# Performance work log

Measured on AMD Instinct MI355X. Metric: run time of the kernel, lower is better.

The kernel has to match this reference:

```python
import jax, jax.numpy as jnp
import numpy as np

EPSILON = 8.0        # Gibbs kernel temperature (JCPOTConfig.epsilon)
NUM_INNER_ITER = 10  # Sinkhorn u/v fixed-point iterations
STAB = 1e-8          # denominator stabilizer, matches torch code


def _cost_matrix(s, t):
    # Euclidean pairwise distance, same math as torch.norm(s[:,None]-t[None,:], dim=2)
    # computed without materializing the [n_s, n_t, d] tensor.
    sq = jnp.sum(s * s, axis=1)[:, None] + jnp.sum(t * t, axis=1)[None, :] - 2.0 * (s @ t.T)
    return jnp.sqrt(jnp.maximum(sq, 0.0))


def setup_inputs() -> dict:
    key = jax.random.key(0)
    k1, k2 = jax.random.split(key)
    return {
        "source_features": jax.random.normal(k1, (4096, 512), dtype=jnp.float32),
        "target_features": jax.random.normal(k2, (4096, 512), dtype=jnp.float32),
    }


def reference(source_features, target_features):
    n_s = source_features.shape[0]
    n_t = target_features.shape[0]
    C = _cost_matrix(source_features, target_features)   # [n_s, n_t]
    K = jnp.exp(-C / EPSILON)                             # Gibbs kernel

    # uniform marginals (JCPOT passes uniform weights; Sinkhorn renormalizes -> same)
    a = jnp.full((n_s, 1), 1.0 / n_s, dtype=C.dtype)
    b = jnp.full((n_t, 1), 1.0 / n_t, dtype=C.dtype)

    def body(carry, _):
        u, v = carry
        u = a / (K @ v + STAB)
        v = b / (K.T @ u + STAB)
        return (u, v), None

    u0 = jnp.ones((n_s, 1), dtype=C.dtype)
    v0 = jnp.ones((n_t, 1), dtype=C.dtype)
    (u, v), _ = jax.lax.scan(body, (u0, v0), None, length=NUM_INNER_ITER)

    coupling = u * K * v.T                                # [n_s, n_t]
    ot_loss = jnp.sum(coupling * C) / (n_s * n_t)         # reduction='mean'
    # returns same contents as the torch dict: ot_loss, coupling, cost_matrix
    return ot_loss, coupling, C
```

## Files before the change

### kernel.cpp

```cpp
#include <hip/hip_runtime.h>
#include <math.h>


#define N_S 4096
#define N_T 4096
#define DIM 512
#define STAB 1e-8f

typedef _Float16 f16x2 __attribute__((ext_vector_type(2)));
typedef _Float16 f16x4 __attribute__((ext_vector_type(4)));
typedef _Float16 f16x8 __attribute__((ext_vector_type(8)));
typedef float f32x4v __attribute__((ext_vector_type(4)));

__global__ __launch_bounds__(256) void k_norms(const float4* __restrict__ S4,
                                               const float4* __restrict__ T4,
                                               float* __restrict__ ns, float* __restrict__ nt) {
    int t = threadIdx.x;
    int lane = t & 63, wave = t >> 6;
    int wid = blockIdx.x * 4 + wave;
    const float4* src; float* dst; int row;
    if (wid < N_S) { src = S4; dst = ns; row = wid; }
    else           { src = T4; dst = nt; row = wid - N_S; }
    float acc = 0.f;
#pragma unroll
    for (int c = 0; c < 2; ++c) {
        float4 x = src[row * 128 + c * 64 + lane];
        acc += x.x*x.x + x.y*x.y + x.z*x.z + x.w*x.w;
    }
#pragma unroll
    for (int m = 32; m; m >>= 1) acc += __shfl_xor(acc, m);
    if (lane == 0) dst[row] = acc;
}

__global__ void k_init(float* v, float* vacc, double* lossd) {
    int g = blockIdx.x * 256 + threadIdx.x;
    if (g < N_T) { v[g] = 1.0f; vacc[g] = 0.0f; }
    if (g == 0) *lossd = 0.0;
}

template<int MODE>
__global__ __launch_bounds__(256) void k_gemm(const float* __restrict__ S, const float* __restrict__ T,
                                              const float* __restrict__ ns, const float* __restrict__ nt,
                                              float* __restrict__ outK, _Float16* __restrict__ outKh,
                                              float* __restrict__ outC) {
    __shared__ _Float16 As[128 * 40];
    __shared__ _Float16 Bs[128 * 40];
    int t = threadIdx.x;
    int lane = t & 63, wave = t >> 6;
    int wr = wave >> 1, wc = wave & 1;
    int brow = blockIdx.x * 128, bcol = blockIdx.y * 128;

    f32x4v acc[4][4] = {};

    for (int kt = 0; kt < DIM; kt += 32) {
        __syncthreads();
#pragma unroll
        for (int w = 0; w < 4; ++w) {
            int e = w * 1024 + t * 4;
            int row = e >> 5, col = e & 31;
            float4 a = *(const float4*)(S + (size_t)(brow + row) * DIM + kt + col);
            f16x4 ah = { (_Float16)a.x, (_Float16)a.y, (_Float16)a.z, (_Float16)a.w };
            *(f16x4*)(&As[row * 40 + col]) = ah;
            float4 b = *(const float4*)(T + (size_t)(bcol + row) * DIM + kt + col);
            f16x4 bh = { (_Float16)b.x, (_Float16)b.y, (_Float16)b.z, (_Float16)b.w };
            *(f16x4*)(&Bs[row * 40 + col]) = bh;
        }
        __syncthreads();

        f16x8 af[4], bf[4];
#pragma unroll
        for (int m = 0; m < 4; ++m)
            af[m] = *(const f16x8*)(&As[(wr * 64 + m * 16 + (lane & 15)) * 40 + (lane >> 4) * 8]);
#pragma unroll
        for (int n = 0; n < 4; ++n)
            bf[n] = *(const f16x8*)(&Bs[(wc * 64 + n * 16 + (lane & 15)) * 40 + (lane >> 4) * 8]);
#pragma unroll
        for (int m = 0; m < 4; ++m)
#pragma unroll
            for (int n = 0; n < 4; ++n)
                acc[m][n] = __builtin_amdgcn_mfma_f32_16x16x32_f16(af[m], bf[n], acc[m][n], 0, 0, 0);
    }

#pragma unroll
    for (int m = 0; m < 4; ++m) {
#pragma unroll
        for (int n = 0; n < 4; ++n) {
#pragma unroll
            for (int r = 0; r < 4; ++r) {
                int i = brow + wr * 64 + m * 16 + (lane >> 4) * 4 + r;
                int j = bcol + wc * 64 + n * 16 + (lane & 15);
                float dot = acc[m][n][r];
                float sq = ns[i] + nt[j] - 2.0f * dot;
                float c = sqrtf(fmaxf(sq, 0.0f));
                float k = __expf(-c * 0.125f);
                size_t idx = (size_t)i * N_T + j;
                outC[idx] = c;
                if constexpr (MODE == 0) outK[idx] = k;
                else                     outKh[idx] = (_Float16)k;
            }
        }
    }
}

__global__ __launch_bounds__(256) void k_sink(const _Float16* __restrict__ Kh,
                                              const float* __restrict__ v,
                                              float* __restrict__ u_out,
                                              float* __restrict__ part) {
    __shared__ _Float16 rows[4][4096];
    __shared__ float u_s[4];
    int t = threadIdx.x, lane = t & 63, w = t >> 6;
    float2 acc[8];
#pragma unroll
    for (int s = 0; s < 8; ++s) acc[s] = make_float2(0.f, 0.f);

    for (int c = 0; c < 2; ++c) {
        if (c) __syncthreads();
        int row = blockIdx.x * 8 + c * 4 + w;
        const _Float16* Kr = Kh + (size_t)row * N_T;
        float dot = 0.f;
#pragma unroll
        for (int it = 0; it < 8; ++it) {
            int j0 = it * 512 + lane * 8;
            f16x8 kv = *(const f16x8*)(Kr + j0);
            float4 v0 = *(const float4*)(v + j0);
            float4 v1 = *(const float4*)(v + j0 + 4);
            *(f16x8*)(&rows[w][j0]) = kv;
            dot += (float)kv[0]*v0.x + (float)kv[1]*v0.y + (float)kv[2]*v0.z + (float)kv[3]*v0.w
                 + (float)kv[4]*v1.x + (float)kv[5]*v1.y + (float)kv[6]*v1.z + (float)kv[7]*v1.w;
        }
#pragma unroll
        for (int m = 32; m; m >>= 1) dot += __shfl_xor(dot, m);
        if (lane == 0) {
            float uv = (1.0f / N_S) / (dot + STAB);
            u_s[w] = uv;
            u_out[row] = uv;
        }
        __syncthreads();
#pragma unroll
        for (int s = 0; s < 8; ++s) {
            int jj = t * 2 + s * 512;
#pragma unroll
            for (int r = 0; r < 4; ++r) {
                f16x2 kk = *(const f16x2*)(&rows[r][jj]);
                float uu = u_s[r];
                acc[s].x += uu * (float)kk[0];
                acc[s].y += uu * (float)kk[1];
            }
        }
    }
    float* pb = part + (size_t)blockIdx.x * N_T;
#pragma unroll
    for (int s = 0; s < 8; ++s)
        *(float2*)(pb + t * 2 + s * 512) = acc[s];
}

__global__ __launch_bounds__(256) void k_vfin2(const float* __restrict__ part, float* __restrict__ v) {
    __shared__ float sums[256];
    int t = threadIdx.x;
    int jl = t & 15, c = t >> 4;
    int j = blockIdx.x * 16 + jl;
    float acc = 0.f;
#pragma unroll 8
    for (int k = 0; k < 32; ++k)
        acc += part[(size_t)(c * 32 + k) * N_T + j];
    sums[t] = acc;
    __syncthreads();
    if (t < 16) {
        float s = 0.f;
#pragma unroll
        for (int c2 = 0; c2 < 16; ++c2) s += sums[c2 * 16 + t];
        v[blockIdx.x * 16 + t] = (1.0f / N_T) / (s + STAB);
    }
}

__global__ __launch_bounds__(256) void k_final2(const _Float16* __restrict__ Kh, const float* __restrict__ Cd,
                                                const float* __restrict__ u, const float* __restrict__ v,
                                                float* __restrict__ W, double* __restrict__ lossd) {
    int t = threadIdx.x, row = blockIdx.x;
    float ui = u[row];
    float lacc = 0.f;
    const _Float16* Kr = Kh + (size_t)row * N_T;
    const float* Cr = Cd + (size_t)row * N_T;
    float* Wr = W + (size_t)row * N_T;
#pragma unroll
    for (int cc = 0; cc < 4; ++cc) {
        int j = (cc * 256 + t) * 4;
        f16x4 kk = *(const f16x4*)(Kr + j);
        float4 c4 = *(const float4*)(Cr + j);
        float4 v4 = *(const float4*)(v + j);
        float4 w4;
        w4.x = ui * (float)kk[0] * v4.x;
        w4.y = ui * (float)kk[1] * v4.y;
        w4.z = ui * (float)kk[2] * v4.z;
        w4.w = ui * (float)kk[3] * v4.w;
        *(float4*)(Wr + j) = w4;
        lacc += w4.x*c4.x + w4.y*c4.y + w4.z*c4.z + w4.w*c4.w;
    }
#pragma unroll
    for (int m = 32; m; m >>= 1) lacc += __shfl_xor(lacc, m);
    __shared__ float wsum[4];
    int lane = t & 63, wave = t >> 6;
    if (lane == 0) wsum[wave] = lacc;
    __syncthreads();
    if (t == 0) atomicAdd(lossd, (double)(wsum[0] + wsum[1] + wsum[2] + wsum[3]));
}

__global__ void k_loss(const double* __restrict__ lossd, float* __restrict__ out0) {
    *out0 = (float)(*lossd / ((double)N_S * (double)N_T));
}

__global__ __launch_bounds__(256) void k_rowmv(const float* __restrict__ Kd,
                                               const float* __restrict__ v, float* __restrict__ u) {
    __shared__ float vl[4096];
    int t = threadIdx.x;
#pragma unroll
    for (int c = 0; c < 16; ++c) vl[c * 256 + t] = v[c * 256 + t];
    __syncthreads();
    int lane = t & 63, wave = t >> 6;
    int row = blockIdx.x * 4 + wave;
    const float* Kr = Kd + (size_t)row * N_T;
    float dot = 0.f;
#pragma unroll 8
    for (int c = 0; c < 64; ++c) {
        int j = c * 64 + lane;
        dot += Kr[j] * vl[j];
    }
#pragma unroll
    for (int m = 32; m; m >>= 1) dot += __shfl_xor(dot, m);
    if (lane == 0) u[row] = (1.0f / N_S) / (dot + STAB);
}

__global__ __launch_bounds__(256) void k_colmv(const float* __restrict__ Kd,
                                               const float* __restrict__ u, float* __restrict__ vacc) {
    __shared__ float ul[64];
    int t = threadIdx.x;
    int rc = blockIdx.y;
    if (t < 64) ul[t] = u[rc * 64 + t];
    __syncthreads();
    int j = blockIdx.x * 256 + t;
    const float* Kp = Kd + (size_t)(rc * 64) * N_T + j;
    float acc = 0.f;
#pragma unroll 8
    for (int r = 0; r < 64; ++r) acc += Kp[(size_t)r * N_T] * ul[r];
    atomicAdd(&vacc[j], acc);
}

__global__ void k_vfin(float* v, float* vacc) {
    int j = blockIdx.x * 256 + threadIdx.x;
    v[j] = (1.0f / N_T) / (vacc[j] + STAB);
    vacc[j] = 0.f;
}

__global__ __launch_bounds__(256) void k_final(float* __restrict__ Kd, const float* __restrict__ Cd,
                                               const float* __restrict__ u, const float* __restrict__ v,
                                               double* __restrict__ lossd) {
    int t = threadIdx.x;
    int row = blockIdx.x;
    float ui = u[row];
    float lacc = 0.f;
#pragma unroll 4
    for (int c = 0; c < 16; ++c) {
        int j = c * 256 + t;
        size_t idx = (size_t)row * N_T + j;
        float w = ui * Kd[idx] * v[j];
        Kd[idx] = w;
        lacc += w * Cd[idx];
    }
#pragma unroll
    for (int m = 32; m; m >>= 1) lacc += __shfl_xor(lacc, m);
    __shared__ float wsum[4];
    int lane = t & 63, wave = t >> 6;
    if (lane == 0) wsum[wave] = lacc;
    __syncthreads();
    if (t == 0) atomicAdd(lossd, (double)(wsum[0] + wsum[1] + wsum[2] + wsum[3]));
}

extern "C" void kernel_launch(void* const* d_in, const int* in_sizes, int n_in,
                              void* d_out, int out_size, void* d_ws, size_t ws_size,
                              hipStream_t stream) {
    const float* S = (const float*)d_in[0];
    const float* T = (const float*)d_in[1];
    float* out = (float*)d_out;
    float* outCoup = out + 1;
    float* outC = out + 1 + (size_t)N_S * N_T;

    const size_t KH_BYTES = (size_t)N_S * N_T * 2;
    const size_t PART_BYTES = (size_t)512 * N_T * 4;
    const size_t need = KH_BYTES + PART_BYTES + 4 * 16384 + 16;

    if (ws_size >= need) {
        _Float16* kh = (_Float16*)d_ws;
        float* part = (float*)((char*)d_ws + KH_BYTES);
        float* ns = (float*)((char*)d_ws + KH_BYTES + PART_BYTES);
        float* nt = ns + 4096;
        float* u  = nt + 4096;
        float* v  = u + 4096;
        double* lossd = (double*)(v + 4096);

        k_norms<<<2048, 256, 0, stream>>>((const float4*)S, (const float4*)T, ns, nt);
        k_init<<<16, 256, 0, stream>>>(v, part, lossd);
        k_gemm<1><<<dim3(32, 32), 256, 0, stream>>>(S, T, ns, nt, nullptr, kh, outC);
        for (int it = 0; it < 10; ++it) {
            k_sink<<<512, 256, 0, stream>>>(kh, v, u, part);
            k_vfin2<<<256, 256, 0, stream>>>(part, v);
        }
        k_final2<<<4096, 256, 0, stream>>>(kh, outC, u, v, outCoup, lossd);
        k_loss<<<1, 1, 0, stream>>>(lossd, out);
    } else {
        float* outK = outCoup;
        float* ws   = (float*)d_ws;
        float* ns   = ws;
        float* nt   = ws + 4096;
        float* u    = ws + 8192;
        float* v    = ws + 12288;
        float* vacc = ws + 16384;
        double* lossd = (double*)(ws + 20480);

        k_norms<<<2048, 256, 0, stream>>>((const float4*)S, (const float4*)T, ns, nt);
        k_init<<<16, 256, 0, stream>>>(v, vacc, lossd);
        k_gemm<0><<<dim3(32, 32), 256, 0, stream>>>(S, T, ns, nt, outK, nullptr, outC);
        for (int it = 0; it < 10; ++it) {
            k_rowmv<<<1024, 256, 0, stream>>>(outK, v, u);
            k_colmv<<<dim3(16, 64), 256, 0, stream>>>(outK, u, vacc);
            k_vfin<<<16, 256, 0, stream>>>(v, vacc);
        }
        k_final<<<4096, 256, 0, stream>>>(outK, outC, u, v, lossd);
        k_loss<<<1, 1, 0, stream>>>(lossd, out);
    }
}
```

Measured before the change: 389.8 us.

## Pre-convert inputs to fp16 tiles, split exp pass, retile Sinkhorn, recompute C from K

Inputs are now converted once to fp16 in a k-tiled layout, so the GEMM loads contiguous half tiles instead of converting fp32 in every block. The GEMM writes only C, and a separate pass computes the fp16 K from C. Sinkhorn now uses 1024 blocks of 4 rows with float4 partial sums, and the reduction reads 64 partials per thread. The final kernel no longer reads C; it rebuilds C from log2 of the fp16 K, which cuts 64MB of reads but adds a 64MB C re-read in the exp pass and loses loss precision.

```diff
diff --git a/kernel.cpp b/kernel.cpp
--- a/kernel.cpp
+++ b/kernel.cpp
@@ -7,10 +7,11 @@
 #define DIM 512
 #define STAB 1e-8f
 
-typedef _Float16 f16x2 __attribute__((ext_vector_type(2)));
 typedef _Float16 f16x4 __attribute__((ext_vector_type(4)));
 typedef _Float16 f16x8 __attribute__((ext_vector_type(8)));
 typedef float f32x4v __attribute__((ext_vector_type(4)));
+
+#define SINK_BLOCKS 1024
 
 __global__ __launch_bounds__(256) void k_norms(const float4* __restrict__ S4,
                                                const float4* __restrict__ T4,
@@ -32,17 +33,212 @@
     if (lane == 0) dst[row] = acc;
 }
 
+__global__ __launch_bounds__(256) void k_cvt(const float* __restrict__ S, const float* __restrict__ T,
+                                             _Float16* __restrict__ Sh2, _Float16* __restrict__ Th2) {
+    int g = blockIdx.x * 256 + threadIdx.x;
+    const float* src; _Float16* dst;
+    if (g < 262144) { src = S; dst = Sh2; }
+    else            { src = T; dst = Th2; g -= 262144; }
+    int row = g >> 6, cb = (g & 63) * 8;
+    float4 x0 = *(const float4*)(src + (size_t)row * 512 + cb);
+    float4 x1 = *(const float4*)(src + (size_t)row * 512 + cb + 4);
+    f16x8 h = { (_Float16)x0.x, (_Float16)x0.y, (_Float16)x0.z, (_Float16)x0.w,
+                (_Float16)x1.x, (_Float16)x1.y, (_Float16)x1.z, (_Float16)x1.w };
+    *(f16x8*)(dst + ((size_t)(cb >> 5) * 4096 + row) * 32 + (cb & 31)) = h;
+}
+
 __global__ void k_init(float* v, float* vacc, double* lossd) {
     int g = blockIdx.x * 256 + threadIdx.x;
     if (g < N_T) { v[g] = 1.0f; vacc[g] = 0.0f; }
     if (g == 0) *lossd = 0.0;
 }
 
-template<int MODE>
-__global__ __launch_bounds__(256) void k_gemm(const float* __restrict__ S, const float* __restrict__ T,
-                                              const float* __restrict__ ns, const float* __restrict__ nt,
-                                              float* __restrict__ outK, _Float16* __restrict__ outKh,
-                                              float* __restrict__ outC) {
+__global__ __launch_bounds__(256) void k_gemm16(const _Float16* __restrict__ Sh2,
+                                                const _Float16* __restrict__ Th2,
+                                                const float* __restrict__ ns,
+                                                const float* __restrict__ nt,
+                                                float* __restrict__ outC) {
+    __shared__ _Float16 As[128 * 40];
+    __shared__ _Float16 Bs[128 * 40];
+    int t = threadIdx.x;
+    int lane = t & 63, wave = t >> 6;
+    int wr = wave >> 1, wc = wave & 1;
+    int brow = blockIdx.x * 128, bcol = blockIdx.y * 128;
+
+    f32x4v acc[4][4] = {};
+
+    for (int kt = 0; kt < 16; ++kt) {
+        __syncthreads();
+        const _Float16* Ab = Sh2 + ((size_t)kt * 4096 + brow) * 32;
+        const _Float16* Bb = Th2 + ((size_t)kt * 4096 + bcol) * 32;
+#pragma unroll
+        for (int w = 0; w < 2; ++w) {
+            int e = w * 2048 + t * 8, row = e >> 5, col = e & 31;
+            *(f16x8*)(&As[row * 40 + col]) = *(const f16x8*)(Ab + row * 32 + col);
+            *(f16x8*)(&Bs[row * 40 + col]) = *(const f16x8*)(Bb + row * 32 + col);
+        }
+        __syncthreads();
+
+        f16x8 af[4], bf[4];
+#pragma unroll
+        for (int m = 0; m < 4; ++m)
+            af[m] = *(const f16x8*)(&As[(wr * 64 + m * 16 + (lane & 15)) * 40 + (lane >> 4) * 8]);
+#pragma unroll
+        for (int n = 0; n < 4; ++n)
+            bf[n] = *(const f16x8*)(&Bs[(wc * 64 + n * 16 + (lane & 15)) * 40 + (lane >> 4) * 8]);
+#pragma unroll
+        for (int m = 0; m < 4; ++m)
+#pragma unroll
+            for (int n = 0; n < 4; ++n)
+                acc[m][n] = __builtin_amdgcn_mfma_f32_16x16x32_f16(af[m], bf[n], acc[m][n], 0, 0, 0);
+    }
+
+#pragma unroll
+    for (int m = 0; m < 4; ++m) {
+#pragma unroll
+        for (int n = 0; n < 4; ++n) {
+#pragma unroll
+            for (int r = 0; r < 4; ++r) {
+                int i = brow + wr * 64 + m * 16 + (lane >> 4) * 4 + r;
+                int j = bcol + wc * 64 + n * 16 + (lane & 15);
+                float sq = ns[i] + nt[j] - 2.0f * acc[m][n][r];
+                outC[(size_t)i * N_T + j] = sqrtf(fmaxf(sq, 0.0f));
+            }
+        }
+    }
+}
+
+__global__ __launch_bounds__(256) void k_kh(const float* __restrict__ Cd, _Float16* __restrict__ Kh) {
+    size_t i = ((size_t)blockIdx.x * 256 + threadIdx.x) * 8;
+    float4 c0 = *(const float4*)(Cd + i);
+    float4 c1 = *(const float4*)(Cd + i + 4);
+    f16x8 h;
+    h[0] = (_Float16)__expf(c0.x * -0.125f);
+    h[1] = (_Float16)__expf(c0.y * -0.125f);
+    h[2] = (_Float16)__expf(c0.z * -0.125f);
+    h[3] = (_Float16)__expf(c0.w * -0.125f);
+    h[4] = (_Float16)__expf(c1.x * -0.125f);
+    h[5] = (_Float16)__expf(c1.y * -0.125f);
+    h[6] = (_Float16)__expf(c1.z * -0.125f);
+    h[7] = (_Float16)__expf(c1.w * -0.125f);
+    *(f16x8*)(Kh + i) = h;
+}
+
+__global__ __launch_bounds__(256) void k_sink2(const _Float16* __restrict__ Kh,
+                                               const float* __restrict__ v,
+                                               float* __restrict__ u_out,
+                                               float* __restrict__ part) {
+    __shared__ _Float16 rows[4][4096];
+    __shared__ float u_s[4];
+    int t = threadIdx.x, lane = t & 63, w = t >> 6;
+    int row = blockIdx.x * 4 + w;
+    const _Float16* Kr = Kh + (size_t)row * N_T;
+
+    f16x8 kk[8];
+#pragma unroll
+    for (int it = 0; it < 8; ++it)
+        kk[it] = *(const f16x8*)(Kr + it * 512 + lane * 8);
+
+    float dot = 0.f;
+#pragma unroll
+    for (int it = 0; it < 8; ++it) {
+        int j0 = it * 512 + lane * 8;
+        float4 v0 = *(const float4*)(v + j0);
+        float4 v1 = *(const float4*)(v + j0 + 4);
+        *(f16x8*)(&rows[w][j0]) = kk[it];
+        dot += (float)kk[it][0]*v0.x + (float)kk[it][1]*v0.y
+             + (float)kk[it][2]*v0.z + (float)kk[it][3]*v0.w
+             + (float)kk[it][4]*v1.x + (float)kk[it][5]*v1.y
+             + (float)kk[it][6]*v1.z + (float)kk[it][7]*v1.w;
+    }
+#pragma unroll
+    for (int m = 32; m; m >>= 1) dot += __shfl_xor(dot, m);
+    if (lane == 0) {
+        float uv = (1.0f / N_S) / (dot + STAB);
+        u_s[w] = uv;
+        u_out[row] = uv;
+    }
+    __syncthreads();
+
+    float4 acc[4] = {};
+#pragma unroll
+    for (int s = 0; s < 4; ++s) {
+        int jj = t * 4 + s * 1024;
+#pragma unroll
+        for (int r = 0; r < 4; ++r) {
+            f16x4 k4 = *(const f16x4*)(&rows[r][jj]);
+            float uu = u_s[r];
+            acc[s].x += uu * (float)k4[0];
+            acc[s].y += uu * (float)k4[1];
+            acc[s].z += uu * (float)k4[2];
+            acc[s].w += uu * (float)k4[3];
+        }
+    }
+    float* pb = part + (size_t)blockIdx.x * N_T;
+#pragma unroll
+    for (int s = 0; s < 4; ++s)
+        *(float4*)(pb + t * 4 + s * 1024) = acc[s];
+}
+
+__global__ __launch_bounds__(256) void k_vred(const float* __restrict__ part, float* __restrict__ v) {
+    __shared__ float sums[256];
+    int t = threadIdx.x;
+    int c = t & 15, p0 = t >> 4;
+    int j = blockIdx.x * 16 + c;
+    float acc = 0.f;
+#pragma unroll 8
+    for (int k = 0; k < 64; ++k)
+        acc += part[(size_t)(p0 * 64 + k) * N_T + j];
+    sums[t] = acc;
+    __syncthreads();
+    if (t < 16) {
+        float s = 0.f;
+#pragma unroll
+        for (int c2 = 0; c2 < 16; ++c2) s += sums[c2 * 16 + t];
+        v[blockIdx.x * 16 + t] = (1.0f / N_T) / (s + STAB);
+    }
+}
+
+__global__ __launch_bounds__(256) void k_final3(const _Float16* __restrict__ Kh,
+                                                const float* __restrict__ u, const float* __restrict__ v,
+                                                float* __restrict__ W, double* __restrict__ lossd) {
+    int t = threadIdx.x, row = blockIdx.x;
+    float ui = u[row];
+    float lacc = 0.f;
+    const float NEG8LN2 = -5.5451774444795623f;
+    const _Float16* Kr = Kh + (size_t)row * N_T;
+    float* Wr = W + (size_t)row * N_T;
+#pragma unroll
+    for (int cc = 0; cc < 4; ++cc) {
+        int j = (cc * 256 + t) * 4;
+        f16x4 kk = *(const f16x4*)(Kr + j);
+        float4 v4 = *(const float4*)(v + j);
+        float4 w4;
+        float kf0 = (float)kk[0], kf1 = (float)kk[1], kf2 = (float)kk[2], kf3 = (float)kk[3];
+        w4.x = ui * kf0 * v4.x;
+        w4.y = ui * kf1 * v4.y;
+        w4.z = ui * kf2 * v4.z;
+        w4.w = ui * kf3 * v4.w;
+        *(float4*)(Wr + j) = w4;
+        lacc += w4.x * (NEG8LN2 * __log2f(kf0)) + w4.y * (NEG8LN2 * __log2f(kf1))
+              + w4.z * (NEG8LN2 * __log2f(kf2)) + w4.w * (NEG8LN2 * __log2f(kf3));
+    }
+#pragma unroll
+    for (int m = 32; m; m >>= 1) lacc += __shfl_xor(lacc, m);
+    __shared__ float wsum[4];
+    int lane = t & 63, wave = t >> 6;
+    if (lane == 0) wsum[wave] = lacc;
+    __syncthreads();
+    if (t == 0) atomicAdd(lossd, (double)(wsum[0] + wsum[1] + wsum[2] + wsum[3]));
+}
+
+__global__ void k_loss(const double* __restrict__ lossd, float* __restrict__ out0) {
+    *out0 = (float)(*lossd / ((double)N_S * (double)N_T));
+}
+
+__global__ __launch_bounds__(256) void k_gemm0(const float* __restrict__ S, const float* __restrict__ T,
+                                               const float* __restrict__ ns, const float* __restrict__ nt,
+                                               float* __restrict__ outK, float* __restrict__ outC) {
     __shared__ _Float16 As[128 * 40];
     __shared__ _Float16 Bs[128 * 40];
     int t = threadIdx.x;
@@ -89,124 +285,14 @@
             for (int r = 0; r < 4; ++r) {
                 int i = brow + wr * 64 + m * 16 + (lane >> 4) * 4 + r;
                 int j = bcol + wc * 64 + n * 16 + (lane & 15);
-                float dot = acc[m][n][r];
-                float sq = ns[i] + nt[j] - 2.0f * dot;
+                float sq = ns[i] + nt[j] - 2.0f * acc[m][n][r];
                 float c = sqrtf(fmaxf(sq, 0.0f));
-                float k = __expf(-c * 0.125f);
                 size_t idx = (size_t)i * N_T + j;
                 outC[idx] = c;
-                if constexpr (MODE == 0) outK[idx] = k;
-                else                     outKh[idx] = (_Float16)k;
+                outK[idx] = __expf(-c * 0.125f);
             }
         }
     }
-}
-
-__global__ __launch_bounds__(256) void k_sink(const _Float16* __restrict__ Kh,
-                                              const float* __restrict__ v,
-                                              float* __restrict__ u_out,
-                                              float* __restrict__ part) {
-    __shared__ _Float16 rows[4][4096];
-    __shared__ float u_s[4];
-    int t = threadIdx.x, lane = t & 63, w = t >> 6;
-    float2 acc[8];
-#pragma unroll
-    for (int s = 0; s < 8; ++s) acc[s] = make_float2(0.f, 0.f);
-
-    for (int c = 0; c < 2; ++c) {
-        if (c) __syncthreads();
-        int row = blockIdx.x * 8 + c * 4 + w;
-        const _Float16* Kr = Kh + (size_t)row * N_T;
-        float dot = 0.f;
-#pragma unroll
-        for (int it = 0; it < 8; ++it) {
-            int j0 = it * 512 + lane * 8;
-            f16x8 kv = *(const f16x8*)(Kr + j0);
-            float4 v0 = *(const float4*)(v + j0);
-            float4 v1 = *(const float4*)(v + j0 + 4);
-            *(f16x8*)(&rows[w][j0]) = kv;
-            dot += (float)kv[0]*v0.x + (float)kv[1]*v0.y + (float)kv[2]*v0.z + (float)kv[3]*v0.w
-                 + (float)kv[4]*v1.x + (float)kv[5]*v1.y + (float)kv[6]*v1.z + (float)kv[7]*v1.w;
-        }
-#pragma unroll
-        for (int m = 32; m; m >>= 1) dot += __shfl_xor(dot, m);
-        if (lane == 0) {
-            float uv = (1.0f / N_S) / (dot + STAB);
-            u_s[w] = uv;
-            u_out[row] = uv;
-        }
-        __syncthreads();
-#pragma unroll
-        for (int s = 0; s < 8; ++s) {
-            int jj = t * 2 + s * 512;
-#pragma unroll
-            for (int r = 0; r < 4; ++r) {
-                f16x2 kk = *(const f16x2*)(&rows[r][jj]);
-                float uu = u_s[r];
-                acc[s].x += uu * (float)kk[0];
-                acc[s].y += uu * (float)kk[1];
-            }
-        }
-    }
-    float* pb = part + (size_t)blockIdx.x * N_T;
-#pragma unroll
-    for (int s = 0; s < 8; ++s)
-        *(float2*)(pb + t * 2 + s * 512) = acc[s];
-}
-
-__global__ __launch_bounds__(256) void k_vfin2(const float* __restrict__ part, float* __restrict__ v) {
-    __shared__ float sums[256];
-    int t = threadIdx.x;
-    int jl = t & 15, c = t >> 4;
-    int j = blockIdx.x * 16 + jl;
-    float acc = 0.f;
-#pragma unroll 8
-    for (int k = 0; k < 32; ++k)
-        acc += part[(size_t)(c * 32 + k) * N_T + j];
-    sums[t] = acc;
-    __syncthreads();
-    if (t < 16) {
-        float s = 0.f;
-#pragma unroll
-        for (int c2 = 0; c2 < 16; ++c2) s += sums[c2 * 16 + t];
-        v[blockIdx.x * 16 + t] = (1.0f / N_T) / (s + STAB);
-    }
-}
-
-__global__ __launch_bounds__(256) void k_final2(const _Float16* __restrict__ Kh, const float* __restrict__ Cd,
-                                                const float* __restrict__ u, const float* __restrict__ v,
-                                                float* __restrict__ W, double* __restrict__ lossd) {
-    int t = threadIdx.x, row = blockIdx.x;
-    float ui = u[row];
-    float lacc = 0.f;
-    const _Float16* Kr = Kh + (size_t)row * N_T;
-    const float* Cr = Cd + (size_t)row * N_T;
-    float* Wr = W + (size_t)row * N_T;
-#pragma unroll
-    for (int cc = 0; cc < 4; ++cc) {
-        int j = (cc * 256 + t) * 4;
-        f16x4 kk = *(const f16x4*)(Kr + j);
-        float4 c4 = *(const float4*)(Cr + j);
-        float4 v4 = *(const float4*)(v + j);
-        float4 w4;
-        w4.x = ui * (float)kk[0] * v4.x;
-        w4.y = ui * (float)kk[1] * v4.y;
-        w4.z = ui * (float)kk[2] * v4.z;
-        w4.w = ui * (float)kk[3] * v4.w;
-        *(float4*)(Wr + j) = w4;
-        lacc += w4.x*c4.x + w4.y*c4.y + w4.z*c4.z + w4.w*c4.w;
-    }
-#pragma unroll
-    for (int m = 32; m; m >>= 1) lacc += __shfl_xor(lacc, m);
-    __shared__ float wsum[4];
-    int lane = t & 63, wave = t >> 6;
-    if (lane == 0) wsum[wave] = lacc;
-    __syncthreads();
-    if (t == 0) atomicAdd(lossd, (double)(wsum[0] + wsum[1] + wsum[2] + wsum[3]));
-}
-
-__global__ void k_loss(const double* __restrict__ lossd, float* __restrict__ out0) {
-    *out0 = (float)(*lossd / ((double)N_S * (double)N_T));
 }
 
 __global__ __launch_bounds__(256) void k_rowmv(const float* __restrict__ Kd,
@@ -284,27 +370,32 @@
     float* outCoup = out + 1;
     float* outC = out + 1 + (size_t)N_S * N_T;
 
-    const size_t KH_BYTES = (size_t)N_S * N_T * 2;
-    const size_t PART_BYTES = (size_t)512 * N_T * 4;
-    const size_t need = KH_BYTES + PART_BYTES + 4 * 16384 + 16;
+    const size_t MB = 1024 * 1024;
+    const size_t need = 56 * MB + 96 * 1024;
 
     if (ws_size >= need) {
-        _Float16* kh = (_Float16*)d_ws;
-        float* part = (float*)((char*)d_ws + KH_BYTES);
-        float* ns = (float*)((char*)d_ws + KH_BYTES + PART_BYTES);
+        char* wsb = (char*)d_ws;
+        _Float16* Sh2 = (_Float16*)wsb;
+        _Float16* Th2 = (_Float16*)(wsb + 4 * MB);
+        _Float16* Kh  = (_Float16*)(wsb + 8 * MB);
+        float* part   = (float*)(wsb + 40 * MB);
+        float* ns = (float*)(wsb + 56 * MB);
         float* nt = ns + 4096;
         float* u  = nt + 4096;
         float* v  = u + 4096;
-        double* lossd = (double*)(v + 4096);
+        float* vacc = v + 4096;
+        double* lossd = (double*)(vacc + 4096);
 
         k_norms<<<2048, 256, 0, stream>>>((const float4*)S, (const float4*)T, ns, nt);
-        k_init<<<16, 256, 0, stream>>>(v, part, lossd);
-        k_gemm<1><<<dim3(32, 32), 256, 0, stream>>>(S, T, ns, nt, nullptr, kh, outC);
+        k_cvt<<<2048, 256, 0, stream>>>(S, T, Sh2, Th2);
+        k_init<<<16, 256, 0, stream>>>(v, vacc, lossd);
+        k_gemm16<<<dim3(32, 32), 256, 0, stream>>>(Sh2, Th2, ns, nt, outC);
+        k_kh<<<8192, 256, 0, stream>>>(outC, Kh);
         for (int it = 0; it < 10; ++it) {
-            k_sink<<<512, 256, 0, stream>>>(kh, v, u, part);
-            k_vfin2<<<256, 256, 0, stream>>>(part, v);
-        }
-        k_final2<<<4096, 256, 0, stream>>>(kh, outC, u, v, outCoup, lossd);
+            k_sink2<<<SINK_BLOCKS, 256, 0, stream>>>(Kh, v, u, part);
+            k_vred<<<256, 256, 0, stream>>>(part, v);
+        }
+        k_final3<<<4096, 256, 0, stream>>>(Kh, u, v, outCoup, lossd);
         k_loss<<<1, 1, 0, stream>>>(lossd, out);
     } else {
         float* outK = outCoup;
@@ -318,7 +409,7 @@
 
         k_norms<<<2048, 256, 0, stream>>>((const float4*)S, (const float4*)T, ns, nt);
         k_init<<<16, 256, 0, stream>>>(v, vacc, lossd);
-        k_gemm<0><<<dim3(32, 32), 256, 0, stream>>>(S, T, ns, nt, outK, nullptr, outC);
+        k_gemm0<<<dim3(32, 32), 256, 0, stream>>>(S, T, ns, nt, outK, outC);
         for (int it = 0; it < 10; ++it) {
             k_rowmv<<<1024, 256, 0, stream>>>(outK, v, u);
             k_colmv<<<dim3(16, 64), 256, 0, stream>>>(outK, u, vacc);
```

Result: slower. 409.4 us (+5.0%).
